# Performance work log

Measured on AMD Instinct MI355X. Metric: run time of the kernel, lower is better.

## Reference

```python
import jax, jax.numpy as jnp
import numpy as np

B, S, D, H = 8, 4096, 512, 8
DK = D // H
DFF = 2 * D
KS = 3          # depthwise conv kernel size
EPS = 1e-6      # linear attention eps
LN_EPS = 1e-5


def setup_inputs() -> dict:
    key = jax.random.key(0)
    ks = jax.random.split(key, 24)
    w = lambda k, shape, s=0.02: (jax.random.normal(k, shape) * s).astype(jnp.float32)
    return {
        "x": jax.random.normal(ks[0], (B, S, D), dtype=jnp.float32),
        # q/k/v/o projections (torch Linear: y = x @ W.T + b, W is [out, in])
        "wq": w(ks[1], (D, D)), "bq": w(ks[2], (D,)),
        "wk": w(ks[3], (D, D)), "bk": w(ks[4], (D,)),
        "wv": w(ks[5], (D, D)), "bv": w(ks[6], (D,)),
        "wo": w(ks[7], (D, D)), "bo": w(ks[8], (D,)),
        # depthwise spatial convs on head_dim channels, weight [DK, KS], bias [DK]
        "qcw": w(ks[9], (DK, KS)), "qcb": w(ks[10], (DK,)),
        "kcw": w(ks[11], (DK, KS)), "kcb": w(ks[12], (DK,)),
        "vcw": w(ks[13], (DK, KS)), "vcb": w(ks[14], (DK,)),
        # conv-FFN 1x1 convs == linears, W1 [DFF, D], W2 [D, DFF]
        "w1": w(ks[15], (DFF, D)), "b1": w(ks[16], (DFF,)),
        "w2": w(ks[17], (D, DFF)), "b2": w(ks[18], (D,)),
        # layer norms
        "ln1_g": jnp.ones((D,), jnp.float32), "ln1_b": jnp.zeros((D,), jnp.float32),
        "ln2_g": jnp.ones((D,), jnp.float32), "ln2_b": jnp.zeros((D,), jnp.float32),
    }


def _sdwc(x, w, b):
    # x: [B, S, H, DK]; causal depthwise conv over seq per channel
    # (torch pads both sides by KS-1 then trims the last KS-1 => left pad only)
    s = x.shape[1]
    xp = jnp.pad(x, ((0, 0), (KS - 1, 0), (0, 0), (0, 0)))
    y = sum(xp[:, j:j + s] * w[:, j] for j in range(KS))
    return y + b


def _ln(x, g, b):
    m = jnp.mean(x, axis=-1, keepdims=True)
    v = jnp.mean((x - m) ** 2, axis=-1, keepdims=True)
    return (x - m) * jax.lax.rsqrt(v + LN_EPS) * g + b


def reference(x, wq, bq, wk, bk, wv, bv, qcw, qcb, kcw, kcb, vcw, vcb,
              wo, bo, w1, b1, w2, b2, ln1_g, ln1_b, ln2_g, ln2_b):
    b_, s_, _ = x.shape
    q = (jnp.einsum('bsd,od->bso', x, wq) + bq).reshape(b_, s_, H, DK)
    k = (jnp.einsum('bsd,od->bso', x, wk) + bk).reshape(b_, s_, H, DK)
    v = (jnp.einsum('bsd,od->bso', x, wv) + bv).reshape(b_, s_, H, DK)
    # depthwise spatial conv + elu(x)+1 feature map on q, k
    q = jax.nn.elu(_sdwc(q, qcw, qcb)) + 1.0
    k = jax.nn.elu(_sdwc(k, kcw, kcb)) + 1.0
    v = _sdwc(v, vcw, vcb)
    # linear attention in [B, H, S, DK]
    Q = q.transpose(0, 2, 1, 3)
    K = k.transpose(0, 2, 1, 3)
    V = v.transpose(0, 2, 1, 3)
    KV = jnp.einsum('bhsd,bhse->bhde', K, V)                       # [B,H,DK,DK]
    Z = 1.0 / jnp.einsum('bhsd,bhd->bhs', Q, K.sum(axis=2) + EPS)  # [B,H,S]
    Vn = jnp.einsum('bhde,bhsd,bhs->bhse', KV, Q, Z)               # [B,H,S,DK]
    attn = Vn.transpose(0, 2, 1, 3).reshape(b_, s_, D)
    attn = jnp.einsum('bsd,od->bso', attn, wo) + bo
    x = _ln(x + attn, ln1_g, ln1_b)
    # conv-FFN with squared (exact) GELU; dropout is identity at eval
    h = jnp.einsum('bsd,cd->bsc', x, w1) + b1
    g = jax.nn.gelu(h, approximate=False)
    h = g * g
    h = jnp.einsum('bsc,dc->bsd', h, w2) + b2
    return _ln(x + h, ln2_g, ln2_b)
```

## Files before the change

kernel.cpp:

```cpp
#include <hip/hip_runtime.h>
#include <hip/hip_bf16.h>
#include <math.h>

#define B_ 8
#define S_ 4096
#define D_ 512
#define H_ 8
#define DK_ 64
#define DFF_ 1024
#define SPLIT_ 16
#define KVSZ_ 4160
#define EPS_ 1e-6f
#define LN_EPS_ 1e-5f

typedef __attribute__((ext_vector_type(8))) short bf16x8;
typedef __attribute__((ext_vector_type(4))) float f32x4;

static __device__ __forceinline__ float b2f(unsigned short u) {
  unsigned int x = ((unsigned int)u) << 16;
  return __builtin_bit_cast(float, x);
}
static __device__ __forceinline__ unsigned short f2b(float f) {
  unsigned int u = __builtin_bit_cast(unsigned int, f);
  u += 0x7FFFu + ((u >> 16) & 1u);
  return (unsigned short)(u >> 16);
}
static __device__ __forceinline__ float elu1(float v) {
  return (v > 0.0f) ? (v + 1.0f) : expf(v);
}

__global__ __launch_bounds__(256) void cvt_f32_bf16(
    const float* __restrict__ in, unsigned short* __restrict__ out, int n8)
{
  const int i = blockIdx.x * 256 + threadIdx.x;
  if (i >= n8) return;
  f32x4 a = ((const f32x4*)in)[i * 2];
  f32x4 b = ((const f32x4*)in)[i * 2 + 1];
  bf16x8 o;
  #pragma unroll
  for (int e = 0; e < 4; ++e) { o[e] = (short)f2b(a[e]); o[e + 4] = (short)f2b(b[e]); }
  ((bf16x8*)out)[i] = o;
}

__global__ __launch_bounds__(256) void cvt_weights(
    const float* __restrict__ wq, const float* __restrict__ wk,
    const float* __restrict__ wv, const float* __restrict__ wo,
    const float* __restrict__ w1, const float* __restrict__ w2,
    const float* __restrict__ bq, const float* __restrict__ bk,
    const float* __restrict__ bv,
    unsigned short* __restrict__ wb, float* __restrict__ bqkv)
{
  const int i = blockIdx.x * 256 + threadIdx.x;
  const float* src; int rel;
  if (i < 65536)       { src = (i < 32768)  ? wq : wk; rel = i & 32767; }
  else if (i < 131072) { src = (i < 98304)  ? wv : wo; rel = (i - 65536) & 32767; }
  else                 { src = (i < 196608) ? w1 : w2; rel = (i - 131072) & 65535; }
  f32x4 a = ((const f32x4*)src)[rel * 2];
  f32x4 b = ((const f32x4*)src)[rel * 2 + 1];
  bf16x8 o;
  #pragma unroll
  for (int e = 0; e < 4; ++e) { o[e] = (short)f2b(a[e]); o[e + 4] = (short)f2b(b[e]); }
  ((bf16x8*)wb)[i] = o;
  if (i < 1536) bqkv[i] = (i < 512) ? bq[i] : (i < 1024 ? bk[i - 512] : bv[i - 1024]);
}

template<int EPI>
__global__ __launch_bounds__(256, 2) void gemm_bt(
    const unsigned short* __restrict__ A,
    const unsigned short* __restrict__ W,
    const float* __restrict__ bias,
    unsigned short* __restrict__ C,
    int M, int N, int K, int ntx)
{
  __shared__ unsigned short sA[3 * 128 * 32];
  __shared__ unsigned short sB[3 * 256 * 32];
  const int t = threadIdx.x;
  const int wave = t >> 6;
  const int lane = t & 63;
  const int bid = blockIdx.x;
  const int logical = (bid & 7) * ((int)gridDim.x >> 3) + (bid >> 3);
  const int row0 = (logical / ntx) << 7;
  const int col0 = (logical % ntx) << 8;

  f32x4 acc[4][8] = {};

  const int srow = (wave << 4) + (lane >> 2);
  const int scol = (lane & 3) << 3;
  const unsigned short* ga = A + (size_t)(row0 + srow) * K + scol;
  const unsigned short* gb = W + (size_t)(col0 + srow) * K + scol;
  const int ldsoff = (wave << 9);

  const int wm = (wave >> 1) << 6;
  const int wn = (wave & 1) << 7;
  const int fr = lane & 15;
  const int fk = (lane >> 4) << 3;

  #define STAGE(bufsel, kt)                                                     \
    {                                                                           \
      _Pragma("unroll")                                                         \
      for (int i = 0; i < 2; ++i)                                               \
        __builtin_amdgcn_global_load_lds(                                       \
            (const __attribute__((address_space(1))) void*)(ga + (size_t)(i * 64) * K + (kt)), \
            (__attribute__((address_space(3))) void*)(sA + (bufsel) * 4096 + i * 2048 + ldsoff), \
            16, 0, 0);                                                          \
      _Pragma("unroll")                                                         \
      for (int i = 0; i < 4; ++i)                                               \
        __builtin_amdgcn_global_load_lds(                                       \
            (const __attribute__((address_space(1))) void*)(gb + (size_t)(i * 64) * K + (kt)), \
            (__attribute__((address_space(3))) void*)(sB + (bufsel) * 8192 + i * 2048 + ldsoff), \
            16, 0, 0);                                                          \
    }

  const int nt = K >> 5;
  STAGE(0, 0);
  STAGE(1, 32);

  int cur = 0, nxt = 2;
  for (int kt = 0; kt < nt; ++kt) {
    __builtin_amdgcn_s_barrier();
    asm volatile("" ::: "memory");
    if (kt + 2 < nt) {
      STAGE(nxt, (kt + 2) * 32);
      nxt = (nxt == 2) ? 0 : nxt + 1;
      asm volatile("s_waitcnt vmcnt(12)" ::: "memory");
    } else if (kt + 1 < nt) {
      asm volatile("s_waitcnt vmcnt(6)" ::: "memory");
    } else {
      asm volatile("s_waitcnt vmcnt(0)" ::: "memory");
    }

    const unsigned short* pA = sA + cur * 4096;
    const unsigned short* pB = sB + cur * 8192;
    bf16x8 af[4], bfv[8];
    #pragma unroll
    for (int i = 0; i < 4; ++i)
      af[i] = *(const bf16x8*)(pA + (wm + i * 16 + fr) * 32 + fk);
    #pragma unroll
    for (int j = 0; j < 8; ++j)
      bfv[j] = *(const bf16x8*)(pB + (wn + j * 16 + fr) * 32 + fk);
    #pragma unroll
    for (int i = 0; i < 4; ++i)
      #pragma unroll
      for (int j = 0; j < 8; ++j)
        acc[i][j] = __builtin_amdgcn_mfma_f32_16x16x32_bf16(af[i], bfv[j], acc[i][j], 0, 0, 0);

    cur = (cur == 2) ? 0 : cur + 1;
  }
  #undef STAGE

  const int crow0 = row0 + wm + ((lane >> 4) << 2);
  const int ccol0 = col0 + wn + fr;
  unsigned short* Cb = C;
  if (EPI == 2) Cb = C + (size_t)(col0 >> 9) * M * 512;
  const int cstride = (EPI == 2) ? 512 : N;
  #pragma unroll
  for (int j = 0; j < 8; ++j) {
    const int col = ccol0 + j * 16;
    const float bv = bias[col];
    const int lcol = (EPI == 2) ? (col & 511) : col;
    #pragma unroll
    for (int i = 0; i < 4; ++i) {
      #pragma unroll
      for (int r = 0; r < 4; ++r) {
        float v = acc[i][j][r] + bv;
        if (EPI == 1) {
          float g = 0.5f * v * (1.0f + erff(v * 0.70710678118654752f));
          v = g * g;
        }
        Cb[(size_t)(crow0 + i * 16 + r) * cstride + lcol] = f2b(v);
      }
    }
  }
}

__global__ __launch_bounds__(256) void kv_partial(
    const unsigned short* __restrict__ kp,
    const unsigned short* __restrict__ vp,
    const float* __restrict__ kcw, const float* __restrict__ kcb,
    const float* __restrict__ vcw, const float* __restrict__ vcb,
    float* __restrict__ part)
{
  __shared__ float kc[16 * 64];
  __shared__ float vc[16 * 64];
  const int t = threadIdx.x;
  const int bh = blockIdx.x;
  const int b = bh >> 3, h = bh & 7;
  const int s0 = blockIdx.y * (S_ / SPLIT_);
  const int d = t >> 2;
  const int e0 = (t & 3) << 4;
  const int lr = (t & 127) >> 3;
  const int lc = (t & 7) << 3;
  const bool isv = t >= 128;

  const float* cw = isv ? vcw : kcw;
  const float* cb = isv ? vcb : kcb;
  float w0[8], w1[8], w2[8], wb[8];
  #pragma unroll
  for (int i = 0; i < 8; ++i) {
    w0[i] = cw[(lc + i) * 3 + 0];
    w1[i] = cw[(lc + i) * 3 + 1];
    w2[i] = cw[(lc + i) * 3 + 2];
    wb[i] = cb[lc + i];
  }
  const unsigned short* src = isv ? vp : kp;
  float* dstc = isv ? vc : kc;

  float acc[16] = {};
  float ksum = 0.0f;

  for (int chunk = 0; chunk < S_ / SPLIT_; chunk += 16) {
    const int s = s0 + chunk + lr;
    const size_t g = ((size_t)(b * S_ + s)) * D_ + h * 64 + lc;
    bf16x8 r0 = *(const bf16x8*)(src + g);
    bf16x8 r1 = {}, r2 = {};
    if (s >= 1) r1 = *(const bf16x8*)(src + g - D_);
    if (s >= 2) r2 = *(const bf16x8*)(src + g - 2 * D_);
    #pragma unroll
    for (int i = 0; i < 8; ++i) {
      float v = w2[i] * b2f((unsigned short)r0[i])
              + w1[i] * b2f((unsigned short)r1[i])
              + w0[i] * b2f((unsigned short)r2[i]) + wb[i];
      if (!isv) v = elu1(v);
      dstc[lr * 64 + lc + i] = v;
    }
    __syncthreads();
    #pragma unroll 4
    for (int ss = 0; ss < 16; ++ss) {
      const float kd = kc[ss * 64 + d];
      ksum += kd;
      #pragma unroll
      for (int j = 0; j < 16; ++j) acc[j] += kd * vc[ss * 64 + e0 + j];
    }
    __syncthreads();
  }
  float* dst = part + ((size_t)bh * SPLIT_ + blockIdx.y) * KVSZ_;
  #pragma unroll
  for (int j = 0; j < 16; ++j) dst[d * 64 + e0 + j] = acc[j];
  if ((t & 3) == 0) dst[4096 + d] = ksum;
}

__global__ __launch_bounds__(256) void kv_finalize(
    const float* __restrict__ part, float* __restrict__ fin)
{
  const int bh = blockIdx.x;
  for (int idx = threadIdx.x; idx < KVSZ_; idx += 256) {
    float s = 0.0f;
    for (int p = 0; p < SPLIT_; ++p) s += part[((size_t)bh * SPLIT_ + p) * KVSZ_ + idx];
    if (idx >= 4096) s += EPS_;
    fin[(size_t)bh * KVSZ_ + idx] = s;
  }
}

__global__ __launch_bounds__(256) void attn_out(
    const unsigned short* __restrict__ qp,
    const float* __restrict__ qcw, const float* __restrict__ qcb,
    const float* __restrict__ fin,
    unsigned short* __restrict__ attn)
{
  __shared__ float kv[64 * 64];
  __shared__ float ks[64];
  __shared__ float qw[192];
  __shared__ float qb[64];
  const int t = threadIdx.x;
  const int bh = blockIdx.x, b = bh >> 3, h = bh & 7;
  const int s = blockIdx.y * 64 + (t >> 2);
  const int e0 = (t & 3) << 4;

  const float* src = fin + (size_t)bh * KVSZ_;
  for (int i = t; i < 4096; i += 256) kv[i] = src[i];
  if (t < 64) ks[t] = src[4096 + t];
  if (t < 192) qw[t] = qcw[t];
  if (t < 64) qb[t] = qcb[t];
  __syncthreads();

  const unsigned short* qrow = qp + ((size_t)(b * S_ + s)) * D_ + h * 64;
  float q[64];
  #pragma unroll
  for (int i8 = 0; i8 < 8; ++i8) {
    bf16x8 a0 = *(const bf16x8*)(qrow + i8 * 8);
    bf16x8 a1 = {}, a2 = {};
    if (s >= 1) a1 = *(const bf16x8*)(qrow - D_ + i8 * 8);
    if (s >= 2) a2 = *(const bf16x8*)(qrow - 2 * (size_t)D_ + i8 * 8);
    #pragma unroll
    for (int k = 0; k < 8; ++k) {
      const int c = i8 * 8 + k;
      float v = qw[c * 3 + 2] * b2f((unsigned short)a0[k])
              + qw[c * 3 + 1] * b2f((unsigned short)a1[k])
              + qw[c * 3 + 0] * b2f((unsigned short)a2[k]) + qb[c];
      q[c] = elu1(v);
    }
  }
  float zden = 0.0f;
  #pragma unroll
  for (int dd = 0; dd < 64; ++dd) zden += q[dd] * ks[dd];
  const float z = 1.0f / zden;

  float acc[16] = {};
  for (int dd = 0; dd < 64; ++dd) {
    const float qd = q[dd];
    #pragma unroll
    for (int j = 0; j < 16; ++j) acc[j] += qd * kv[dd * 64 + e0 + j];
  }
  unsigned short* orow = attn + ((size_t)(b * S_ + s)) * D_ + h * 64 + e0;
  bf16x8 o0, o1;
  #pragma unroll
  for (int j = 0; j < 8; ++j) { o0[j] = (short)f2b(acc[j] * z); o1[j] = (short)f2b(acc[8 + j] * z); }
  *(bf16x8*)(orow) = o0;
  *(bf16x8*)(orow + 8) = o1;
}

template<bool AF32, bool OF32>
__global__ __launch_bounds__(256) void ln_add(
    const void* __restrict__ xa_,
    const unsigned short* __restrict__ xb,
    const float* __restrict__ gg,
    const float* __restrict__ bb,
    void* __restrict__ out_)
{
  const int t = threadIdx.x, lane = t & 63, w = t >> 6;
  const size_t row = (size_t)blockIdx.x * 4 + w;
  const size_t base = row * D_ + lane * 8;

  float v[8];
  if (AF32) {
    const float* xa = (const float*)xa_;
    f32x4 a0 = *(const f32x4*)(xa + base);
    f32x4 a1 = *(const f32x4*)(xa + base + 4);
    #pragma unroll
    for (int i = 0; i < 4; ++i) { v[i] = a0[i]; v[i + 4] = a1[i]; }
  } else {
    bf16x8 a = *(const bf16x8*)((const unsigned short*)xa_ + base);
    #pragma unroll
    for (int i = 0; i < 8; ++i) v[i] = b2f((unsigned short)a[i]);
  }
  bf16x8 c = *(const bf16x8*)(xb + base);
  float sum = 0.0f;
  #pragma unroll
  for (int i = 0; i < 8; ++i) { v[i] += b2f((unsigned short)c[i]); sum += v[i]; }
  #pragma unroll
  for (int off = 1; off < 64; off <<= 1) sum += __shfl_xor(sum, off, 64);
  const float mean = sum * (1.0f / 512.0f);
  float sq = 0.0f;
  #pragma unroll
  for (int i = 0; i < 8; ++i) { const float dd = v[i] - mean; sq += dd * dd; }
  #pragma unroll
  for (int off = 1; off < 64; off <<= 1) sq += __shfl_xor(sq, off, 64);
  const float rstd = rsqrtf(sq * (1.0f / 512.0f) + LN_EPS_);

  if (OF32) {
    float* out = (float*)out_;
    f32x4 o0, o1;
    #pragma unroll
    for (int i = 0; i < 4; ++i) {
      o0[i] = (v[i] - mean) * rstd * gg[lane * 8 + i] + bb[lane * 8 + i];
      o1[i] = (v[i + 4] - mean) * rstd * gg[lane * 8 + i + 4] + bb[lane * 8 + i + 4];
    }
    *(f32x4*)(out + base) = o0;
    *(f32x4*)(out + base + 4) = o1;
  } else {
    unsigned short* out = (unsigned short*)out_;
    bf16x8 o;
    #pragma unroll
    for (int i = 0; i < 8; ++i)
      o[i] = (short)f2b((v[i] - mean) * rstd * gg[lane * 8 + i] + bb[lane * 8 + i]);
    *(bf16x8*)(out + base) = o;
  }
}

extern "C" void kernel_launch(void* const* d_in, const int* in_sizes, int n_in,
                              void* d_out, int out_size, void* d_ws, size_t ws_size,
                              hipStream_t stream) {
  const float* x    = (const float*)d_in[0];
  const float* wq   = (const float*)d_in[1];
  const float* bq   = (const float*)d_in[2];
  const float* wk   = (const float*)d_in[3];
  const float* bk   = (const float*)d_in[4];
  const float* wv   = (const float*)d_in[5];
  const float* bv   = (const float*)d_in[6];
  const float* wo   = (const float*)d_in[7];
  const float* bo   = (const float*)d_in[8];
  const float* qcw  = (const float*)d_in[9];
  const float* qcb  = (const float*)d_in[10];
  const float* kcw  = (const float*)d_in[11];
  const float* kcb  = (const float*)d_in[12];
  const float* vcw  = (const float*)d_in[13];
  const float* vcb  = (const float*)d_in[14];
  const float* w1   = (const float*)d_in[15];
  const float* b1   = (const float*)d_in[16];
  const float* w2   = (const float*)d_in[17];
  const float* b2   = (const float*)d_in[18];
  const float* ln1g = (const float*)d_in[19];
  const float* ln1b = (const float*)d_in[20];
  const float* ln2g = (const float*)d_in[21];
  const float* ln2b = (const float*)d_in[22];

  const size_t E = (size_t)B_ * S_ * D_;
  unsigned short* s0 = (unsigned short*)d_ws;
  unsigned short* s1 = s0 + E;
  unsigned short* s2 = s0 + 2 * E;
  unsigned short* s3 = s0 + 3 * E;
  float* part = (float*)s3;
  float* fin  = part + (size_t)64 * SPLIT_ * KVSZ_;

  unsigned short* wb = (unsigned short*)d_out;
  unsigned short* wqkv_b = wb;
  unsigned short* wo_b   = wb + 786432;
  unsigned short* w1_b   = wb + 1048576;
  unsigned short* w2_b   = wb + 1572864;
  float* bqkv = (float*)(wb + 2097152);

  const int M = B_ * S_;

  cvt_f32_bf16<<<(int)(E / 8 / 256), 256, 0, stream>>>(x, s3, (int)(E / 8));
  cvt_weights<<<1024, 256, 0, stream>>>(wq, wk, wv, wo, w1, w2, bq, bk, bv, wb, bqkv);

  gemm_bt<2><<<1536, 256, 0, stream>>>(s3, wqkv_b, bqkv, s0, M, 1536, D_, 6);
  kv_partial<<<dim3(B_ * H_, SPLIT_), 256, 0, stream>>>(s1, s2, kcw, kcb, vcw, vcb, part);
  kv_finalize<<<B_ * H_, 256, 0, stream>>>(part, fin);
  attn_out<<<dim3(B_ * H_, S_ / 64), 256, 0, stream>>>(s0, qcw, qcb, fin, s1);
  gemm_bt<0><<<512, 256, 0, stream>>>(s1, wo_b, bo, s2, M, D_, D_, 2);
  ln_add<true, false><<<M / 4, 256, 0, stream>>>(x, s2, ln1g, ln1b, s3);
  gemm_bt<1><<<1024, 256, 0, stream>>>(s3, w1_b, b1, s0, M, DFF_, D_, 4);
  gemm_bt<0><<<512, 256, 0, stream>>>(s0, w2_b, b2, s2, M, D_, DFF_, 2);
  ln_add<false, true><<<M / 4, 256, 0, stream>>>(s3, s2, ln2g, ln2b, d_out);
}
```

Measured before the change: 630.4 us.

## Split Q conv into elementwise kernel and run attention output on MFMA

The fused scalar attn_out kernel is replaced by two kernels. A vectorized dwconv_q kernel computes the Q depthwise conv, elu+1 and the normalizer Z, and writes a bf16 feature map. attn_mm then multiplies Q by the KV matrix using bf16 MFMA instructions with a transposed bf16 KV tile held in LDS. This removes the register-heavy scalar FMA loop, but adds an extra kernel launch and a round trip of Q through memory, and rounds KV to bf16.

```diff
diff --git a/kernel.cpp b/kernel.cpp
--- a/kernel.cpp
+++ b/kernel.cpp
@@ -173,6 +173,57 @@
   }
 }
 
+__global__ __launch_bounds__(256) void dwconv_q(
+    const unsigned short* __restrict__ in,
+    const float* __restrict__ cw,
+    const float* __restrict__ cb,
+    const float* __restrict__ fin,
+    float* __restrict__ zout,
+    unsigned short* __restrict__ out)
+{
+  const int vid = blockIdx.x * 256 + threadIdx.x;
+  const int d8 = vid & 63;
+  const int bs = vid >> 6;
+  const int s  = bs & (S_ - 1);
+  const int d0 = d8 << 3;
+  const int dk0 = d0 & 63;
+  const int h  = d8 >> 3;
+  const int bh = (bs >> 12) * 8 + h;
+
+  float acc[8], wf[3][8];
+  #pragma unroll
+  for (int i = 0; i < 8; ++i) acc[i] = cb[dk0 + i];
+  #pragma unroll
+  for (int j = 0; j < 3; ++j)
+    #pragma unroll
+    for (int i = 0; i < 8; ++i) wf[j][i] = cw[(dk0 + i) * 3 + j];
+
+  const size_t base = (size_t)bs * D_ + d0;
+  #pragma unroll
+  for (int j = 0; j < 3; ++j) {
+    const int sr = s - 2 + j;
+    if (sr >= 0) {
+      bf16x8 xv = *(const bf16x8*)(in + base - (size_t)(2 - j) * D_);
+      #pragma unroll
+      for (int i = 0; i < 8; ++i) acc[i] += wf[j][i] * b2f((unsigned short)xv[i]);
+    }
+  }
+  const float* ksumf = fin + (size_t)bh * KVSZ_ + 4096 + dk0;
+  float part = 0.0f;
+  bf16x8 ov;
+  #pragma unroll
+  for (int i = 0; i < 8; ++i) {
+    const float v = elu1(acc[i]);
+    part += v * ksumf[i];
+    ov[i] = (short)f2b(v);
+  }
+  *(bf16x8*)(out + base) = ov;
+  part += __shfl_xor(part, 1, 64);
+  part += __shfl_xor(part, 2, 64);
+  part += __shfl_xor(part, 4, 64);
+  if ((threadIdx.x & 7) == 0) zout[bs * 8 + h] = 1.0f / part;
+}
+
 __global__ __launch_bounds__(256) void kv_partial(
     const unsigned short* __restrict__ kp,
     const unsigned short* __restrict__ vp,
@@ -251,62 +302,62 @@
   }
 }
 
-__global__ __launch_bounds__(256) void attn_out(
-    const unsigned short* __restrict__ qp,
-    const float* __restrict__ qcw, const float* __restrict__ qcb,
+__global__ __launch_bounds__(256) void attn_mm(
+    const unsigned short* __restrict__ qf,
     const float* __restrict__ fin,
+    const float* __restrict__ z,
     unsigned short* __restrict__ attn)
 {
-  __shared__ float kv[64 * 64];
-  __shared__ float ks[64];
-  __shared__ float qw[192];
-  __shared__ float qb[64];
+  __shared__ unsigned short kvT[64 * 72];
   const int t = threadIdx.x;
-  const int bh = blockIdx.x, b = bh >> 3, h = bh & 7;
-  const int s = blockIdx.y * 64 + (t >> 2);
-  const int e0 = (t & 3) << 4;
-
-  const float* src = fin + (size_t)bh * KVSZ_;
-  for (int i = t; i < 4096; i += 256) kv[i] = src[i];
-  if (t < 64) ks[t] = src[4096 + t];
-  if (t < 192) qw[t] = qcw[t];
-  if (t < 64) qb[t] = qcb[t];
+  const int wave = t >> 6, lane = t & 63;
+  const int h = (int)blockIdx.x & 7;
+  const int m0 = ((int)blockIdx.x >> 3) << 7;
+  const int bh = (m0 >> 12) * 8 + h;
+
+  const float* kvsrc = fin + (size_t)bh * KVSZ_;
+  for (int i = t; i < 4096; i += 256) {
+    const int d = i >> 6, e = i & 63;
+    kvT[e * 72 + d] = f2b(kvsrc[i]);
+  }
   __syncthreads();
 
-  const unsigned short* qrow = qp + ((size_t)(b * S_ + s)) * D_ + h * 64;
-  float q[64];
-  #pragma unroll
-  for (int i8 = 0; i8 < 8; ++i8) {
-    bf16x8 a0 = *(const bf16x8*)(qrow + i8 * 8);
-    bf16x8 a1 = {}, a2 = {};
-    if (s >= 1) a1 = *(const bf16x8*)(qrow - D_ + i8 * 8);
-    if (s >= 2) a2 = *(const bf16x8*)(qrow - 2 * (size_t)D_ + i8 * 8);
-    #pragma unroll
-    for (int k = 0; k < 8; ++k) {
-      const int c = i8 * 8 + k;
-      float v = qw[c * 3 + 2] * b2f((unsigned short)a0[k])
-              + qw[c * 3 + 1] * b2f((unsigned short)a1[k])
-              + qw[c * 3 + 0] * b2f((unsigned short)a2[k]) + qb[c];
-      q[c] = elu1(v);
-    }
-  }
-  float zden = 0.0f;
-  #pragma unroll
-  for (int dd = 0; dd < 64; ++dd) zden += q[dd] * ks[dd];
-  const float z = 1.0f / zden;
-
-  float acc[16] = {};
-  for (int dd = 0; dd < 64; ++dd) {
-    const float qd = q[dd];
-    #pragma unroll
-    for (int j = 0; j < 16; ++j) acc[j] += qd * kv[dd * 64 + e0 + j];
-  }
-  unsigned short* orow = attn + ((size_t)(b * S_ + s)) * D_ + h * 64 + e0;
-  bf16x8 o0, o1;
-  #pragma unroll
-  for (int j = 0; j < 8; ++j) { o0[j] = (short)f2b(acc[j] * z); o1[j] = (short)f2b(acc[8 + j] * z); }
-  *(bf16x8*)(orow) = o0;
-  *(bf16x8*)(orow + 8) = o1;
+  const int fr = lane & 15;
+  const int fk = (lane >> 4) << 3;
+  const int row_w = m0 + wave * 32;
+
+  bf16x8 bfv[4][2];
+  #pragma unroll
+  for (int j = 0; j < 4; ++j)
+    #pragma unroll
+    for (int ks = 0; ks < 2; ++ks)
+      bfv[j][ks] = *(const bf16x8*)(kvT + (j * 16 + fr) * 72 + ks * 32 + fk);
+
+  f32x4 acc[2][4] = {};
+  #pragma unroll
+  for (int i = 0; i < 2; ++i) {
+    #pragma unroll
+    for (int ks = 0; ks < 2; ++ks) {
+      bf16x8 af = *(const bf16x8*)(qf +
+          (size_t)(row_w + i * 16 + fr) * D_ + h * 64 + ks * 32 + fk);
+      #pragma unroll
+      for (int j = 0; j < 4; ++j)
+        acc[i][j] = __builtin_amdgcn_mfma_f32_16x16x32_bf16(af, bfv[j][ks], acc[i][j], 0, 0, 0);
+    }
+  }
+
+  #pragma unroll
+  for (int i = 0; i < 2; ++i) {
+    #pragma unroll
+    for (int r = 0; r < 4; ++r) {
+      const int row = row_w + i * 16 + ((lane >> 4) << 2) + r;
+      const float zz = z[row * 8 + h];
+      unsigned short* orow = attn + (size_t)row * D_ + h * 64 + fr;
+      #pragma unroll
+      for (int j = 0; j < 4; ++j)
+        orow[j * 16] = f2b(acc[i][j][r] * zz);
+    }
+  }
 }
 
 template<bool AF32, bool OF32>
@@ -401,6 +452,7 @@
   unsigned short* s3 = s0 + 3 * E;
   float* part = (float*)s3;
   float* fin  = part + (size_t)64 * SPLIT_ * KVSZ_;
+  float* zbuf = fin + (size_t)64 * KVSZ_;
 
   unsigned short* wb = (unsigned short*)d_out;
   unsigned short* wqkv_b = wb;
@@ -417,8 +469,9 @@
   gemm_bt<2><<<1536, 256, 0, stream>>>(s3, wqkv_b, bqkv, s0, M, 1536, D_, 6);
   kv_partial<<<dim3(B_ * H_, SPLIT_), 256, 0, stream>>>(s1, s2, kcw, kcb, vcw, vcb, part);
   kv_finalize<<<B_ * H_, 256, 0, stream>>>(part, fin);
-  attn_out<<<dim3(B_ * H_, S_ / 64), 256, 0, stream>>>(s0, qcw, qcb, fin, s1);
-  gemm_bt<0><<<512, 256, 0, stream>>>(s1, wo_b, bo, s2, M, D_, D_, 2);
+  dwconv_q<<<M * 64 / 256, 256, 0, stream>>>(s0, qcw, qcb, fin, zbuf, s1);
+  attn_mm<<<(M / 128) * H_, 256, 0, stream>>>(s1, fin, zbuf, s0);
+  gemm_bt<0><<<512, 256, 0, stream>>>(s0, wo_b, bo, s2, M, D_, D_, 2);
   ln_add<true, false><<<M / 4, 256, 0, stream>>>(x, s2, ln1g, ln1b, s3);
   gemm_bt<1><<<1024, 256, 0, stream>>>(s3, w1_b, b1, s0, M, DFF_, D_, 4);
   gemm_bt<0><<<512, 256, 0, stream>>>(s0, w2_b, b2, s2, M, D_, DFF_, 2);
```

Result: faster. 532.7 us (-15.5%).
